# Kernel optimization log

Measured on AMD Instinct MI355X. Metric: run time of the kernel, lower is better.

Reference implementation:

```python
import jax, jax.numpy as jnp
import numpy as np

N_NODES = 100000
N_EDGES = 1600000
D_IN = 128
D_OUT = 128


def setup_inputs() -> dict:
    key = jax.random.key(0)
    k_x, k_r, k_c, k_v, k_w = jax.random.split(key, 5)
    X = jax.random.normal(k_x, (N_NODES, D_IN), dtype=jnp.float32)
    A_rows = jax.random.randint(k_r, (N_EDGES,), 0, N_NODES, dtype=jnp.int32)
    A_cols = jax.random.randint(k_c, (N_EDGES,), 0, N_NODES, dtype=jnp.int32)
    A_vals = jax.random.uniform(k_v, (N_EDGES,), dtype=jnp.float32)
    # Xavier-uniform linear weight [out, in], zero bias (matches reset_parameters)
    limit = float(np.sqrt(6.0 / (D_IN + D_OUT)))
    W = jax.random.uniform(k_w, (D_OUT, D_IN), dtype=jnp.float32, minval=-limit, maxval=limit)
    b = jnp.zeros((D_OUT,), dtype=jnp.float32)
    return {"X": X, "A_rows": A_rows, "A_cols": A_cols, "A_vals": A_vals, "W": W, "b": b}


def reference(X, A_rows, A_cols, A_vals, W, b):
    # h = A_sparse @ X  (COO SpMM: gather neighbor features, scale, scatter-add by row)
    msgs = A_vals[:, None] * X[A_cols]          # [E, D_IN]
    h = jax.ops.segment_sum(msgs, A_rows, num_segments=N_NODES)  # [N, D_IN]
    # dense linear projection
    return h @ W.T + b
```

## Files before the change

### kernel.cpp

```cpp
#include <hip/hip_runtime.h>

#define N_NODES_C 100000
#define N_EDGES_C 1600000
#define D_C 128
#define NBKT 1563
#define RPB 64
#define CAP 1536
#define PTILE 8192
#define NPB ((N_EDGES_C + PTILE - 1) / PTILE)
#define GROWS 128
#define NGB ((N_NODES_C + GROWS - 1) / GROWS)
#define WB_STRIDE 136

static __device__ __forceinline__ unsigned short f2bf(float x) {
    unsigned u = __float_as_uint(x);
    unsigned r = 0x7fffu + ((u >> 16) & 1u);
    return (unsigned short)((u + r) >> 16);
}
static __device__ __forceinline__ float bflo(unsigned u) { return __uint_as_float(u << 16); }
static __device__ __forceinline__ float bfhi(unsigned u) { return __uint_as_float(u & 0xffff0000u); }

typedef __attribute__((ext_vector_type(8))) __bf16 bf16x8;
typedef __attribute__((ext_vector_type(4))) float f32x4;
union FragU { uint4 u; bf16x8 b; };

__global__ __launch_bounds__(256) void prep(const float* __restrict__ W,
                                            const float* __restrict__ b,
                                            unsigned short* __restrict__ Wbf,
                                            int* __restrict__ gcount,
                                            float* __restrict__ pbias) {
    int t = blockIdx.x * 256 + threadIdx.x;
    if (t < 2048) {
        int lane = t & 63;
        int fs = (t >> 6) & 3;
        int tt = t >> 8;
        const float* src = W + (tt * 16 + (lane & 15)) * D_C + fs * 32 + (lane >> 4) * 8;
        float4 w0 = *(const float4*)(src);
        float4 w1 = *(const float4*)(src + 4);
        uint4 v;
        v.x = (unsigned)f2bf(w0.x) | ((unsigned)f2bf(w0.y) << 16);
        v.y = (unsigned)f2bf(w0.z) | ((unsigned)f2bf(w0.w) << 16);
        v.z = (unsigned)f2bf(w1.x) | ((unsigned)f2bf(w1.y) << 16);
        v.w = (unsigned)f2bf(w1.z) | ((unsigned)f2bf(w1.w) << 16);
        *(uint4*)&Wbf[t * 8] = v;
    } else if (t < 2048 + NBKT) {
        gcount[t - 2048] = 0;
    } else {
        int k = t - (2048 + NBKT);
        if (k < 128) pbias[k] = b[(k & 7) * 16 + (k >> 3)];
    }
}

union SMemF {
    struct {
        int lhist[NBKT];
        int lbase[NBKT];
    } part;
    unsigned short wb[16384];
};

__global__ __launch_bounds__(256) void fused(const float* __restrict__ X,
                                             const int* __restrict__ rows,
                                             const int* __restrict__ cols,
                                             const float* __restrict__ vals,
                                             const unsigned short* __restrict__ Wbf,
                                             int* __restrict__ gcount,
                                             int2* __restrict__ staging,
                                             unsigned short* __restrict__ Y,
                                             int n, int E) {
    __shared__ SMemF sm;
    const int tid = threadIdx.x;

    if (blockIdx.x < NPB) {
        const int t0 = blockIdx.x * PTILE;

        for (int i = tid; i < NBKT; i += 256) sm.part.lhist[i] = 0;
        __syncthreads();

        unsigned ebr[PTILE / 256];
#pragma unroll
        for (int k = 0; k < PTILE / 256; ++k) {
            int e = t0 + k * 256 + tid;
            if (e < E) {
                int r = rows[e];
                int bkt = r >> 6;
                int rnk = atomicAdd(&sm.part.lhist[bkt], 1);
                ebr[k] = ((unsigned)bkt << 19) | ((unsigned)(r & 63) << 13) | (unsigned)rnk;
            }
        }
        __syncthreads();

        for (int i = tid; i < NBKT; i += 256)
            sm.part.lbase[i] = sm.part.lhist[i] ? atomicAdd(&gcount[i], sm.part.lhist[i]) : 0;
        __syncthreads();

#pragma unroll
        for (int k = 0; k < PTILE / 256; ++k) {
            int e = t0 + k * 256 + tid;
            if (e < E) {
                int bkt = ebr[k] >> 19;
                int dst = sm.part.lbase[bkt] + (int)(ebr[k] & 0x1FFFu);
                if (dst < CAP) {
                    int rl = (ebr[k] >> 13) & 63;
                    int2 p;
                    p.x = cols[e] | (rl << 17);
                    p.y = __float_as_int(vals[e]);
                    staging[(long)bkt * CAP + dst] = p;
                }
            }
        }
        return;
    }

    const int g = blockIdx.x - NPB;
    const int wave = tid >> 6;
    const int lane = tid & 63;
    const int m16 = lane & 15;
    const int quad = lane >> 4;

    for (int i = tid; i < 2048; i += 256)
        *(uint4*)&sm.wb[i * 8] = *(const uint4*)&Wbf[i * 8];

    const int grow0 = g * GROWS;

    FragU a[4];
    {
        int row = grow0 + wave * 16 + m16;
        int rowc = (row < n) ? row : (n - 1);
        const float* xp = X + (long)rowc * D_C + quad * 8;
#pragma unroll
        for (int s = 0; s < 4; ++s) {
            float4 x0 = *(const float4*)(xp + s * 32);
            float4 x1 = *(const float4*)(xp + s * 32 + 4);
            a[s].u.x = (unsigned)f2bf(x0.x) | ((unsigned)f2bf(x0.y) << 16);
            a[s].u.y = (unsigned)f2bf(x0.z) | ((unsigned)f2bf(x0.w) << 16);
            a[s].u.z = (unsigned)f2bf(x1.x) | ((unsigned)f2bf(x1.y) << 16);
            a[s].u.w = (unsigned)f2bf(x1.z) | ((unsigned)f2bf(x1.w) << 16);
        }
    }
    __syncthreads();

#pragma unroll
    for (int rt = 0; rt < 2; ++rt) {
        const int row0 = grow0 + rt * 64 + wave * 16;
        if (rt) {
            int row = row0 + m16;
            int rowc = (row < n) ? row : (n - 1);
            const float* xp = X + (long)rowc * D_C + quad * 8;
#pragma unroll
            for (int s = 0; s < 4; ++s) {
                float4 x0 = *(const float4*)(xp + s * 32);
                float4 x1 = *(const float4*)(xp + s * 32 + 4);
                a[s].u.x = (unsigned)f2bf(x0.x) | ((unsigned)f2bf(x0.y) << 16);
                a[s].u.y = (unsigned)f2bf(x0.z) | ((unsigned)f2bf(x0.w) << 16);
                a[s].u.z = (unsigned)f2bf(x1.x) | ((unsigned)f2bf(x1.y) << 16);
                a[s].u.w = (unsigned)f2bf(x1.z) | ((unsigned)f2bf(x1.w) << 16);
            }
        }

        f32x4 acc[8];
#pragma unroll
        for (int t = 0; t < 8; ++t) acc[t] = (f32x4){0.f, 0.f, 0.f, 0.f};

#pragma unroll
        for (int s = 0; s < 4; ++s) {
#pragma unroll
            for (int t = 0; t < 8; ++t) {
                FragU bf;
                bf.u = *(const uint4*)&sm.wb[(((t * 4 + s) * 64) + lane) * 8];
                acc[t] = __builtin_amdgcn_mfma_f32_16x16x32_bf16(a[s].b, bf.b, acc[t], 0, 0, 0);
            }
        }

#pragma unroll
        for (int r = 0; r < 4; ++r) {
            int orow = row0 + quad * 4 + r;
            if (orow < n) {
                uint4 v;
                v.x = (unsigned)f2bf(acc[0][r]) | ((unsigned)f2bf(acc[1][r]) << 16);
                v.y = (unsigned)f2bf(acc[2][r]) | ((unsigned)f2bf(acc[3][r]) << 16);
                v.z = (unsigned)f2bf(acc[4][r]) | ((unsigned)f2bf(acc[5][r]) << 16);
                v.w = (unsigned)f2bf(acc[6][r]) | ((unsigned)f2bf(acc[7][r]) << 16);
                *(uint4*)&Y[(long)orow * D_C + m16 * 8] = v;
            }
        }
    }
}

__global__ __launch_bounds__(256) void sort_aggregate(const int* __restrict__ gcount,
                                                      const int2* __restrict__ staging,
                                                      const unsigned short* __restrict__ Y,
                                                      const float* __restrict__ pbias,
                                                      float* __restrict__ out, int n) {
    __shared__ int2 pl[CAP];
    __shared__ int hist[RPB];
    __shared__ int lcur[RPB];
    __shared__ int rbegL[RPB];
    __shared__ int rcntL[RPB];

    const int bb = blockIdx.x, tid = threadIdx.x;
    int cnt = gcount[bb];
    if (cnt > CAP) cnt = CAP;
    const long s = (long)bb * CAP;

    if (tid < RPB) hist[tid] = 0;
    __syncthreads();

    int2 p_reg[6];
#pragma unroll
    for (int k = 0; k < 6; ++k) {
        int i = k * 256 + tid;
        if (i < cnt) p_reg[k] = staging[s + i];
    }
#pragma unroll
    for (int k = 0; k < 6; ++k) {
        int i = k * 256 + tid;
        if (i < cnt) atomicAdd(&hist[((unsigned)p_reg[k].x) >> 17], 1);
    }
    __syncthreads();

    int v = (tid < RPB) ? hist[tid] : 0;
    for (int off = 1; off < RPB; off <<= 1) {
        int t = (tid >= off && tid < RPB) ? hist[tid - off] : 0;
        __syncthreads();
        if (tid < RPB) hist[tid] += t;
        __syncthreads();
    }
    if (tid < RPB) {
        int excl = hist[tid] - v;
        lcur[tid] = excl;
        rbegL[tid] = excl;
        rcntL[tid] = v;
    }
    __syncthreads();

#pragma unroll
    for (int k = 0; k < 6; ++k) {
        int i = k * 256 + tid;
        if (i < cnt) {
            int rl = ((unsigned)p_reg[k].x) >> 17;
            int slot = atomicAdd(&lcur[rl], 1);
            pl[slot] = p_reg[k];
        }
    }
    __syncthreads();

    const int lane = tid & 15;
    const unsigned short* Yl = Y + lane * 8;
    float4 b0 = *(const float4*)&pbias[lane * 8];
    float4 b1 = *(const float4*)&pbias[lane * 8 + 4];

#pragma unroll
    for (int pass = 0; pass < RPB / 16; ++pass) {
        int rlocal = pass * 16 + (tid >> 4);
        int row = bb * RPB + rlocal;
        if (row >= n) continue;

        int i = rbegL[rlocal];
        int e = i + rcntL[rlocal];

        float acc[8];
        acc[0] = b0.x; acc[1] = b0.y; acc[2] = b0.z; acc[3] = b0.w;
        acc[4] = b1.x; acc[5] = b1.y; acc[6] = b1.z; acc[7] = b1.w;

        for (; i + 8 <= e; i += 8) {
            int2 p[8];
            uint4 y[8];
#pragma unroll
            for (int u = 0; u < 8; ++u) p[u] = pl[i + u];
#pragma unroll
            for (int u = 0; u < 8; ++u)
                y[u] = *(const uint4*)&Yl[(long)(p[u].x & 0x1FFFF) * D_C];
#pragma unroll
            for (int u = 0; u < 8; ++u) {
                float v2 = __int_as_float(p[u].y);
                acc[0] += v2 * bflo(y[u].x); acc[1] += v2 * bfhi(y[u].x);
                acc[2] += v2 * bflo(y[u].y); acc[3] += v2 * bfhi(y[u].y);
                acc[4] += v2 * bflo(y[u].z); acc[5] += v2 * bfhi(y[u].z);
                acc[6] += v2 * bflo(y[u].w); acc[7] += v2 * bfhi(y[u].w);
            }
        }
        for (; i + 4 <= e; i += 4) {
            int2 p[4];
            uint4 y[4];
#pragma unroll
            for (int u = 0; u < 4; ++u) p[u] = pl[i + u];
#pragma unroll
            for (int u = 0; u < 4; ++u)
                y[u] = *(const uint4*)&Yl[(long)(p[u].x & 0x1FFFF) * D_C];
#pragma unroll
            for (int u = 0; u < 4; ++u) {
                float v2 = __int_as_float(p[u].y);
                acc[0] += v2 * bflo(y[u].x); acc[1] += v2 * bfhi(y[u].x);
                acc[2] += v2 * bflo(y[u].y); acc[3] += v2 * bfhi(y[u].y);
                acc[4] += v2 * bflo(y[u].z); acc[5] += v2 * bfhi(y[u].z);
                acc[6] += v2 * bflo(y[u].w); acc[7] += v2 * bfhi(y[u].w);
            }
        }
        for (; i < e; ++i) {
            int2 p = pl[i];
            uint4 y = *(const uint4*)&Yl[(long)(p.x & 0x1FFFF) * D_C];
            float v2 = __int_as_float(p.y);
            acc[0] += v2 * bflo(y.x); acc[1] += v2 * bfhi(y.x);
            acc[2] += v2 * bflo(y.y); acc[3] += v2 * bfhi(y.y);
            acc[4] += v2 * bflo(y.z); acc[5] += v2 * bfhi(y.z);
            acc[6] += v2 * bflo(y.w); acc[7] += v2 * bfhi(y.w);
        }

        float* op = out + (long)row * D_C + lane;
#pragma unroll
        for (int j = 0; j < 8; ++j)
            __builtin_nontemporal_store(acc[j], op + j * 16);
    }
}

__global__ __launch_bounds__(256) void gemm_mfma(const float* __restrict__ X,
                                                 const float* __restrict__ W,
                                                 unsigned short* __restrict__ Y, int n) {
    __shared__ unsigned short Wb[128 * WB_STRIDE];

    const int tid = threadIdx.x;
    const int wave = tid >> 6;
    const int lane = tid & 63;
    const int m16 = lane & 15;
    const int quad = lane >> 4;

    const int row0 = blockIdx.x * 64 + wave * 16;
    int row = row0 + m16;
    int rowc = (row < n) ? row : (n - 1);

    float4 xv[4][2];
    const float* xp = X + (long)rowc * D_C + quad * 8;
#pragma unroll
    for (int s = 0; s < 4; ++s) {
        xv[s][0] = *(const float4*)(xp + s * 32);
        xv[s][1] = *(const float4*)(xp + s * 32 + 4);
    }

    for (int i = tid; i < 128 * 32; i += 256) {
        int o = i >> 5;
        int k4 = (i & 31) * 4;
        float4 w = *(const float4*)&W[o * 128 + k4];
        uint2 p;
        p.x = (unsigned)f2bf(w.x) | ((unsigned)f2bf(w.y) << 16);
        p.y = (unsigned)f2bf(w.z) | ((unsigned)f2bf(w.w) << 16);
        *(uint2*)&Wb[o * WB_STRIDE + k4] = p;
    }
    __syncthreads();

    FragU a[4];
#pragma unroll
    for (int s = 0; s < 4; ++s) {
        a[s].u.x = (unsigned)f2bf(xv[s][0].x) | ((unsigned)f2bf(xv[s][0].y) << 16);
        a[s].u.y = (unsigned)f2bf(xv[s][0].z) | ((unsigned)f2bf(xv[s][0].w) << 16);
        a[s].u.z = (unsigned)f2bf(xv[s][1].x) | ((unsigned)f2bf(xv[s][1].y) << 16);
        a[s].u.w = (unsigned)f2bf(xv[s][1].z) | ((unsigned)f2bf(xv[s][1].w) << 16);
    }

    f32x4 acc[8];
#pragma unroll
    for (int t = 0; t < 8; ++t) acc[t] = (f32x4){0.f, 0.f, 0.f, 0.f};

#pragma unroll
    for (int s = 0; s < 4; ++s) {
#pragma unroll
        for (int t = 0; t < 8; ++t) {
            FragU bf;
            bf.u = *(const uint4*)&Wb[(t * 16 + m16) * WB_STRIDE + s * 32 + quad * 8];
            acc[t] = __builtin_amdgcn_mfma_f32_16x16x32_bf16(a[s].b, bf.b, acc[t], 0, 0, 0);
        }
    }

#pragma unroll
    for (int t = 0; t < 8; ++t) {
#pragma unroll
        for (int r = 0; r < 4; ++r) {
            int orow = row0 + quad * 4 + r;
            if (orow < n) Y[(long)orow * D_C + t * 16 + m16] = f2bf(acc[t][r]);
        }
    }
}

__global__ __launch_bounds__(256) void init_out(const float* __restrict__ b,
                                                float* __restrict__ out, int n) {
    int idx = blockIdx.x * 256 + threadIdx.x;
    int total = n * (D_C / 4);
    if (idx < total) {
        int o4 = idx & (D_C / 4 - 1);
        ((float4*)out)[idx] = ((const float4*)b)[o4];
    }
}

__global__ __launch_bounds__(256) void scatter_edges(const int* __restrict__ rows,
                                                     const int* __restrict__ cols,
                                                     const float* __restrict__ vals,
                                                     const unsigned short* __restrict__ Y,
                                                     float* __restrict__ out, int E) {
    int e = blockIdx.x * 8 + (threadIdx.x >> 5);
    if (e >= E) return;
    int lane = threadIdx.x & 31;
    int row = rows[e];
    int col = cols[e];
    float v = vals[e];
    uint2 y = *(const uint2*)&Y[(long)col * D_C + lane * 4];
    float* dst = out + (long)row * D_C + lane * 4;
    unsafeAtomicAdd(dst + 0, v * bflo(y.x));
    unsafeAtomicAdd(dst + 1, v * bfhi(y.x));
    unsafeAtomicAdd(dst + 2, v * bflo(y.y));
    unsafeAtomicAdd(dst + 3, v * bfhi(y.y));
}

extern "C" void kernel_launch(void* const* d_in, const int* in_sizes, int n_in,
                              void* d_out, int out_size, void* d_ws, size_t ws_size,
                              hipStream_t stream) {
    const float* X  = (const float*)d_in[0];
    const int*   Ar = (const int*)d_in[1];
    const int*   Ac = (const int*)d_in[2];
    const float* Av = (const float*)d_in[3];
    const float* W  = (const float*)d_in[4];
    const float* b  = (const float*)d_in[5];
    float* out = (float*)d_out;

    unsigned short* Y = (unsigned short*)d_ws;
    int2* staging = (int2*)(Y + 12800000);
    unsigned short* Wbf = (unsigned short*)(staging + (size_t)NBKT * CAP);
    int* gcount = (int*)(Wbf + 16384);
    float* pbias = (float*)(gcount + NBKT);
    size_t need = (size_t)12800000 * 2 + (size_t)NBKT * CAP * 8 + 32768 +
                  (size_t)NBKT * 4 + 512;

    if (ws_size >= need) {
        prep<<<15, 256, 0, stream>>>(W, b, Wbf, gcount, pbias);
        fused<<<NPB + NGB, 256, 0, stream>>>(X, Ar, Ac, Av, Wbf, gcount, staging, Y,
                                             N_NODES_C, N_EDGES_C);
        sort_aggregate<<<NBKT, 256, 0, stream>>>(gcount, staging, Y, pbias, out, N_NODES_C);
    } else {
        gemm_mfma<<<(N_NODES_C + 63) / 64, 256, 0, stream>>>(X, W, Y, N_NODES_C);
        init_out<<<(N_NODES_C * (D_C / 4) + 255) / 256, 256, 0, stream>>>(b, out, N_NODES_C);
        scatter_edges<<<(N_EDGES_C + 7) / 8, 256, 0, stream>>>(Ar, Ac, Av, Y, out, N_EDGES_C);
    }
}
```

Baseline: 224.4 us.

## Split fused partition/GEMM kernel into two launches and unroll gather loop to 16

The combined kernel that did both edge partitioning and the bf16 MFMA projection, depending on block index, is split into two separate kernels launched back to back on the same stream. Each now uses only its own shared memory and registers, which may improve occupancy, but it loses the concurrency of both phases running in one grid and adds a launch. Separately, the main gather loop in the aggregation kernel is unrolled from 8 to 16 edges, keeping more loads in flight at the cost of higher register pressure.

```diff
diff --git a/kernel.cpp b/kernel.cpp
--- a/kernel.cpp
+++ b/kernel.cpp
@@ -51,77 +51,67 @@
     }
 }
 
-union SMemF {
-    struct {
-        int lhist[NBKT];
-        int lbase[NBKT];
-    } part;
-    unsigned short wb[16384];
-};
-
-__global__ __launch_bounds__(256) void fused(const float* __restrict__ X,
-                                             const int* __restrict__ rows,
-                                             const int* __restrict__ cols,
-                                             const float* __restrict__ vals,
-                                             const unsigned short* __restrict__ Wbf,
-                                             int* __restrict__ gcount,
-                                             int2* __restrict__ staging,
-                                             unsigned short* __restrict__ Y,
-                                             int n, int E) {
-    __shared__ SMemF sm;
+__global__ __launch_bounds__(256) void partition(const int* __restrict__ rows,
+                                                 const int* __restrict__ cols,
+                                                 const float* __restrict__ vals,
+                                                 int* __restrict__ gcount,
+                                                 int2* __restrict__ staging, int E) {
+    __shared__ int lhist[NBKT];
+    __shared__ int lbase[NBKT];
     const int tid = threadIdx.x;
-
-    if (blockIdx.x < NPB) {
-        const int t0 = blockIdx.x * PTILE;
-
-        for (int i = tid; i < NBKT; i += 256) sm.part.lhist[i] = 0;
-        __syncthreads();
-
-        unsigned ebr[PTILE / 256];
-#pragma unroll
-        for (int k = 0; k < PTILE / 256; ++k) {
-            int e = t0 + k * 256 + tid;
-            if (e < E) {
-                int r = rows[e];
-                int bkt = r >> 6;
-                int rnk = atomicAdd(&sm.part.lhist[bkt], 1);
-                ebr[k] = ((unsigned)bkt << 19) | ((unsigned)(r & 63) << 13) | (unsigned)rnk;
-            }
-        }
-        __syncthreads();
-
-        for (int i = tid; i < NBKT; i += 256)
-            sm.part.lbase[i] = sm.part.lhist[i] ? atomicAdd(&gcount[i], sm.part.lhist[i]) : 0;
-        __syncthreads();
-
-#pragma unroll
-        for (int k = 0; k < PTILE / 256; ++k) {
-            int e = t0 + k * 256 + tid;
-            if (e < E) {
-                int bkt = ebr[k] >> 19;
-                int dst = sm.part.lbase[bkt] + (int)(ebr[k] & 0x1FFFu);
-                if (dst < CAP) {
-                    int rl = (ebr[k] >> 13) & 63;
-                    int2 p;
-                    p.x = cols[e] | (rl << 17);
-                    p.y = __float_as_int(vals[e]);
-                    staging[(long)bkt * CAP + dst] = p;
-                }
-            }
-        }
-        return;
-    }
-
-    const int g = blockIdx.x - NPB;
+    const int t0 = blockIdx.x * PTILE;
+
+    for (int i = tid; i < NBKT; i += 256) lhist[i] = 0;
+    __syncthreads();
+
+    unsigned ebr[PTILE / 256];
+#pragma unroll
+    for (int k = 0; k < PTILE / 256; ++k) {
+        int e = t0 + k * 256 + tid;
+        if (e < E) {
+            int r = rows[e];
+            int bkt = r >> 6;
+            int rnk = atomicAdd(&lhist[bkt], 1);
+            ebr[k] = ((unsigned)bkt << 19) | ((unsigned)(r & 63) << 13) | (unsigned)rnk;
+        }
+    }
+    __syncthreads();
+
+    for (int i = tid; i < NBKT; i += 256)
+        lbase[i] = lhist[i] ? atomicAdd(&gcount[i], lhist[i]) : 0;
+    __syncthreads();
+
+#pragma unroll
+    for (int k = 0; k < PTILE / 256; ++k) {
+        int e = t0 + k * 256 + tid;
+        if (e < E) {
+            int bkt = ebr[k] >> 19;
+            int dst = lbase[bkt] + (int)(ebr[k] & 0x1FFFu);
+            if (dst < CAP) {
+                int rl = (ebr[k] >> 13) & 63;
+                int2 p;
+                p.x = cols[e] | (rl << 17);
+                p.y = __float_as_int(vals[e]);
+                staging[(long)bkt * CAP + dst] = p;
+            }
+        }
+    }
+}
+
+__global__ __launch_bounds__(256) void gemm(const float* __restrict__ X,
+                                            const unsigned short* __restrict__ Wbf,
+                                            unsigned short* __restrict__ Y, int n) {
+    __shared__ unsigned short wb[16384];
+    const int tid = threadIdx.x;
     const int wave = tid >> 6;
     const int lane = tid & 63;
     const int m16 = lane & 15;
     const int quad = lane >> 4;
 
     for (int i = tid; i < 2048; i += 256)
-        *(uint4*)&sm.wb[i * 8] = *(const uint4*)&Wbf[i * 8];
-
-    const int grow0 = g * GROWS;
+        *(uint4*)&wb[i * 8] = *(const uint4*)&Wbf[i * 8];
+
+    const int grow0 = blockIdx.x * GROWS;
 
     FragU a[4];
     {
@@ -167,7 +157,7 @@
 #pragma unroll
             for (int t = 0; t < 8; ++t) {
                 FragU bf;
-                bf.u = *(const uint4*)&sm.wb[(((t * 4 + s) * 64) + lane) * 8];
+                bf.u = *(const uint4*)&wb[(((t * 4 + s) * 64) + lane) * 8];
                 acc[t] = __builtin_amdgcn_mfma_f32_16x16x32_bf16(a[s].b, bf.b, acc[t], 0, 0, 0);
             }
         }
@@ -263,16 +253,16 @@
         acc[0] = b0.x; acc[1] = b0.y; acc[2] = b0.z; acc[3] = b0.w;
         acc[4] = b1.x; acc[5] = b1.y; acc[6] = b1.z; acc[7] = b1.w;
 
-        for (; i + 8 <= e; i += 8) {
-            int2 p[8];
-            uint4 y[8];
-#pragma unroll
-            for (int u = 0; u < 8; ++u) p[u] = pl[i + u];
-#pragma unroll
-            for (int u = 0; u < 8; ++u)
+        for (; i + 16 <= e; i += 16) {
+            int2 p[16];
+            uint4 y[16];
+#pragma unroll
+            for (int u = 0; u < 16; ++u) p[u] = pl[i + u];
+#pragma unroll
+            for (int u = 0; u < 16; ++u)
                 y[u] = *(const uint4*)&Yl[(long)(p[u].x & 0x1FFFF) * D_C];
 #pragma unroll
-            for (int u = 0; u < 8; ++u) {
+            for (int u = 0; u < 16; ++u) {
                 float v2 = __int_as_float(p[u].y);
                 acc[0] += v2 * bflo(y[u].x); acc[1] += v2 * bfhi(y[u].x);
                 acc[2] += v2 * bflo(y[u].y); acc[3] += v2 * bfhi(y[u].y);
@@ -431,8 +421,8 @@
 
     if (ws_size >= need) {
         prep<<<15, 256, 0, stream>>>(W, b, Wbf, gcount, pbias);
-        fused<<<NPB + NGB, 256, 0, stream>>>(X, Ar, Ac, Av, Wbf, gcount, staging, Y,
-                                             N_NODES_C, N_EDGES_C);
+        partition<<<NPB, 256, 0, stream>>>(Ar, Ac, Av, gcount, staging, N_EDGES_C);
+        gemm<<<NGB, 256, 0, stream>>>(X, Wbf, Y, N_NODES_C);
         sort_aggregate<<<NBKT, 256, 0, stream>>>(gcount, staging, Y, pbias, out, N_NODES_C);
     } else {
         gemm_mfma<<<(N_NODES_C + 63) / 64, 256, 0, stream>>>(X, W, Y, N_NODES_C);
```

Result: slower. 229.4 us (+2.2%).
